# Performance work log

Measured on AMD Instinct MI355X. Metric: run time of the kernel, lower is better.

The kernel has to match this reference:

```python
import jax, jax.numpy as jnp
import numpy as np


def setup_inputs() -> dict:
    key = jax.random.key(0)
    k1, k2 = jax.random.split(key)
    B, S, D = 32, 1024, 384
    MAX_MEL_LEN = 8192  # >= max possible sum of durations (7*1024)
    x = jax.random.normal(k1, (B, S, D), dtype=jnp.float32)
    duration = jax.random.randint(k2, (B, S), 0, 8, dtype=jnp.int32)
    return {"x": x, "duration": duration, "max_mel_len": MAX_MEL_LEN}


def reference(x, duration, max_mel_len):
    # x: (B, S, D) float, duration: (B, S) int, max_mel_len: python int
    B, S, D = x.shape
    csum = jnp.cumsum(duration, axis=1)          # (B, S) inclusive cumsum
    mel_len = csum[:, -1]                        # (B,) expanded length per sample
    t = jnp.arange(max_mel_len, dtype=csum.dtype)  # (T,) output frame indices
    # frame t maps to token i where csum[i-1] <= t < csum[i]; side='right'
    # correctly skips zero-duration tokens (repeated csum values)
    idx = jax.vmap(lambda c: jnp.searchsorted(c, t, side='right'))(csum)  # (B, T)
    idx = jnp.clip(idx, 0, S - 1)
    out = jnp.take_along_axis(x, idx[:, :, None], axis=1)  # (B, T, D) gather
    mask = t[None, :] < mel_len[:, None]                   # (B, T) pad mask
    out = out * mask[:, :, None].astype(x.dtype)
    return out, mel_len.astype(jnp.int64)
```

## Files before the change

### kernel.cpp

```cpp
#include <hip/hip_runtime.h>


#define BATCH 32
#define SRC_S 1024
#define DIM   384
#define ROWS  32
#define C4    (DIM / 4)
#define NXCD  8

typedef float f32x4 __attribute__((ext_vector_type(4)));
typedef int   i32x4 __attribute__((ext_vector_type(4)));

__global__ __launch_bounds__(256)
void lr_fused_kernel(const f32x4* __restrict__ x4,
                     const int* __restrict__ duration,
                     f32x4* __restrict__ out4,
                     float* __restrict__ mel_out, int T) {
    __shared__ int wsum[4];
    __shared__ int src[ROWS];

    const int l = blockIdx.x;
    const int xcd = l & (NXCD - 1);
    const int j = l >> 3;
    const int b = xcd + NXCD * (j >> 8);
    const int t0 = (j & 255) * ROWS;
    const int tid = threadIdx.x;
    const int lane = tid & 63;
    const int wid = tid >> 6;

    if (tid < ROWS) src[tid] = -1;

    const i32x4 d = ((const i32x4*)(duration + b * SRC_S))[tid];
    const int s0 = d.x;
    const int s1 = s0 + d.y;
    const int s2 = s1 + d.z;
    const int s3 = s2 + d.w;
    int tot = s3;
    #pragma unroll
    for (int off = 1; off < 64; off <<= 1) {
        const int n = __shfl_up(tot, off, 64);
        if (lane >= off) tot += n;
    }
    if (lane == 63) wsum[wid] = tot;
    __syncthreads();
    int base = 0;
    #pragma unroll
    for (int w = 0; w < 3; ++w) base += (w < wid) ? wsum[w] : 0;
    const int mel_len = wsum[0] + wsum[1] + wsum[2] + wsum[3];
    const int pre = base + tot - s3;

    const int cs[4] = {pre + s0, pre + s1, pre + s2, pre + s3};
    const int st[4] = {pre, pre + s0, pre + s1, pre + s2};
    #pragma unroll
    for (int e = 0; e < 4; ++e) {
        const int lo = (st[e] > t0) ? st[e] : t0;
        const int hi = (cs[e] < t0 + ROWS) ? cs[e] : (t0 + ROWS);
        for (int t = lo; t < hi; ++t) src[t - t0] = tid * 4 + e;
    }
    __syncthreads();

    if (t0 == 0 && tid == 0) mel_out[b] = (float)mel_len;

    const f32x4* __restrict__ xb = x4 + (size_t)b * SRC_S * C4;
    f32x4* __restrict__ ob = out4 + ((size_t)b * T + t0) * C4;

    #pragma unroll
    for (int k = 0; k < (ROWS * C4) / 256; ++k) {
        const int i = tid + k * 256;
        const int row = i / C4;
        const int col = i - row * C4;
        const int sidx = src[row];
        f32x4 v = (f32x4)(0.f);
        if (sidx >= 0) v = xb[(size_t)sidx * C4 + col];
        __builtin_nontemporal_store(v, &ob[i]);
    }
}

extern "C" void kernel_launch(void* const* d_in, const int* in_sizes, int n_in,
                              void* d_out, int out_size, void* d_ws, size_t ws_size,
                              hipStream_t stream) {
    const float* x = (const float*)d_in[0];
    const int* duration = (const int*)d_in[1];
    const int T = (out_size - BATCH) / (BATCH * DIM);

    float* out = (float*)d_out;
    float* mel_out = out + (size_t)BATCH * T * DIM;

    const int nblocks = BATCH * (T / ROWS);
    lr_fused_kernel<<<nblocks, 256, 0, stream>>>((const f32x4*)x, duration,
                                                 (f32x4*)out, mel_out, T);
}
```

Measured before the change: 438.0 us.

## Split cumsum into separate kernel and skip padded tiles in gather

A small pre-kernel now computes the per-batch cumulative durations and mel lengths once, storing them in device globals. Previously every output tile redid the full 1024-element scan. The gather kernel reads the precomputed csum, writes zeros for tiles entirely past mel_len without any scan or sync, and stores precomputed row offsets in shared memory. Rows per block double to 64. The cost is an extra kernel launch and a global-memory round trip for csum. The block-to-batch mapping also hardcodes T=8192.

```diff
diff --git a/kernel.cpp b/kernel.cpp
--- a/kernel.cpp
+++ b/kernel.cpp
@@ -4,31 +4,23 @@
 #define BATCH 32
 #define SRC_S 1024
 #define DIM   384
-#define ROWS  32
+#define ROWS  64
 #define C4    (DIM / 4)
 #define NXCD  8
 
 typedef float f32x4 __attribute__((ext_vector_type(4)));
 typedef int   i32x4 __attribute__((ext_vector_type(4)));
 
+__device__ int g_csum[BATCH * SRC_S];
+__device__ int g_mel[BATCH];
+
 __global__ __launch_bounds__(256)
-void lr_fused_kernel(const f32x4* __restrict__ x4,
-                     const int* __restrict__ duration,
-                     f32x4* __restrict__ out4,
-                     float* __restrict__ mel_out, int T) {
+void lr_csum_kernel(const int* __restrict__ duration, float* __restrict__ mel_out) {
     __shared__ int wsum[4];
-    __shared__ int src[ROWS];
-
-    const int l = blockIdx.x;
-    const int xcd = l & (NXCD - 1);
-    const int j = l >> 3;
-    const int b = xcd + NXCD * (j >> 8);
-    const int t0 = (j & 255) * ROWS;
+    const int b = blockIdx.x;
     const int tid = threadIdx.x;
     const int lane = tid & 63;
     const int wid = tid >> 6;
-
-    if (tid < ROWS) src[tid] = -1;
 
     const i32x4 d = ((const i32x4*)(duration + b * SRC_S))[tid];
     const int s0 = d.x;
@@ -46,32 +38,68 @@
     int base = 0;
     #pragma unroll
     for (int w = 0; w < 3; ++w) base += (w < wid) ? wsum[w] : 0;
-    const int mel_len = wsum[0] + wsum[1] + wsum[2] + wsum[3];
     const int pre = base + tot - s3;
 
-    const int cs[4] = {pre + s0, pre + s1, pre + s2, pre + s3};
-    const int st[4] = {pre, pre + s0, pre + s1, pre + s2};
+    i32x4 c;
+    c.x = pre + s0; c.y = pre + s1; c.z = pre + s2; c.w = pre + s3;
+    ((i32x4*)(g_csum + b * SRC_S))[tid] = c;
+
+    if (tid == 255) {
+        const int mel = pre + s3;
+        g_mel[b] = mel;
+        mel_out[b] = (float)mel;
+    }
+}
+
+__global__ __launch_bounds__(256)
+void lr_gather_kernel(const f32x4* __restrict__ x4, f32x4* __restrict__ out4, int T) {
+    const int l = blockIdx.x;
+    const int xcd = l & (NXCD - 1);
+    const int j = l >> 3;
+    const int wpb = 8192 / ROWS;
+    const int b = xcd + NXCD * (j >> 7);
+    const int t0 = (j & (wpb - 1)) * ROWS;
+    const int tid = threadIdx.x;
+
+    f32x4* __restrict__ ob = out4 + ((size_t)b * T + t0) * C4;
+    const int mel = g_mel[b];
+
+    if (t0 >= mel) {
+        const f32x4 z = (f32x4)(0.f);
+        #pragma unroll
+        for (int k = 0; k < (ROWS * C4) / 256; ++k)
+            __builtin_nontemporal_store(z, &ob[tid + k * 256]);
+        return;
+    }
+
+    __shared__ int src[ROWS];
+    const int* __restrict__ cb = g_csum + b * SRC_S;
+    const i32x4 c = ((const i32x4*)cb)[tid];
+    const int prev = (tid == 0) ? 0 : cb[4 * tid - 1];
+
+    if (tid < ROWS) src[tid] = -1;
+    __syncthreads();
+
+    const int st[4] = {prev, c.x, c.y, c.z};
+    const int en[4] = {c.x, c.y, c.z, c.w};
     #pragma unroll
     for (int e = 0; e < 4; ++e) {
         const int lo = (st[e] > t0) ? st[e] : t0;
-        const int hi = (cs[e] < t0 + ROWS) ? cs[e] : (t0 + ROWS);
-        for (int t = lo; t < hi; ++t) src[t - t0] = tid * 4 + e;
+        const int hi = (en[e] < t0 + ROWS) ? en[e] : (t0 + ROWS);
+        const int off = (tid * 4 + e) * C4;
+        for (int t = lo; t < hi; ++t) src[t - t0] = off;
     }
     __syncthreads();
 
-    if (t0 == 0 && tid == 0) mel_out[b] = (float)mel_len;
-
     const f32x4* __restrict__ xb = x4 + (size_t)b * SRC_S * C4;
-    f32x4* __restrict__ ob = out4 + ((size_t)b * T + t0) * C4;
-
     #pragma unroll
     for (int k = 0; k < (ROWS * C4) / 256; ++k) {
         const int i = tid + k * 256;
         const int row = i / C4;
         const int col = i - row * C4;
-        const int sidx = src[row];
+        const int o = src[row];
         f32x4 v = (f32x4)(0.f);
-        if (sidx >= 0) v = xb[(size_t)sidx * C4 + col];
+        if (o >= 0) v = xb[o + col];
         __builtin_nontemporal_store(v, &ob[i]);
     }
 }
@@ -86,7 +114,9 @@
     float* out = (float*)d_out;
     float* mel_out = out + (size_t)BATCH * T * DIM;
 
+    lr_csum_kernel<<<BATCH, 256, 0, stream>>>(duration, mel_out);
+
     const int nblocks = BATCH * (T / ROWS);
-    lr_fused_kernel<<<nblocks, 256, 0, stream>>>((const f32x4*)x, duration,
-                                                 (f32x4*)out, mel_out, T);
+    lr_gather_kernel<<<nblocks, 256, 0, stream>>>((const f32x4*)x,
+                                                  (f32x4*)out, T);
 }
```

New measurement: 442.7 us. Within noise of the previous version (+1.1%).

## Split into index-table kernel plus flat gather sweep kernel

Applied to the files above, without the earlier changes.

Replaces the fused kernel, in which every block redoes the full per-batch prefix sum, with two kernels. The first computes the duration cumsum once per batch and writes a global source-offset table. The second does a flat, grid-strided gather sweep with 24 iterations per thread and plain stores instead of nontemporal ones. This removes the redundant per-block scans, at the cost of an extra launch, a global table round-trip, a serial per-thread table fill in only 32 blocks, and the loss of the XCD-aware block mapping.

```diff
diff --git a/kernel.cpp b/kernel.cpp
--- a/kernel.cpp
+++ b/kernel.cpp
@@ -4,31 +4,23 @@
 #define BATCH 32
 #define SRC_S 1024
 #define DIM   384
-#define ROWS  32
 #define C4    (DIM / 4)
-#define NXCD  8
+#define TMAX  8192
+#define NROW  (BATCH * TMAX)
 
 typedef float f32x4 __attribute__((ext_vector_type(4)));
 typedef int   i32x4 __attribute__((ext_vector_type(4)));
 
+__device__ int g_srcoff[NROW];
+
 __global__ __launch_bounds__(256)
-void lr_fused_kernel(const f32x4* __restrict__ x4,
-                     const int* __restrict__ duration,
-                     f32x4* __restrict__ out4,
-                     float* __restrict__ mel_out, int T) {
+void lr_table_kernel(const int* __restrict__ duration, float* __restrict__ mel_out,
+                     int T) {
     __shared__ int wsum[4];
-    __shared__ int src[ROWS];
-
-    const int l = blockIdx.x;
-    const int xcd = l & (NXCD - 1);
-    const int j = l >> 3;
-    const int b = xcd + NXCD * (j >> 8);
-    const int t0 = (j & 255) * ROWS;
+    const int b = blockIdx.x;
     const int tid = threadIdx.x;
     const int lane = tid & 63;
     const int wid = tid >> 6;
-
-    if (tid < ROWS) src[tid] = -1;
 
     const i32x4 d = ((const i32x4*)(duration + b * SRC_S))[tid];
     const int s0 = d.x;
@@ -46,33 +38,38 @@
     int base = 0;
     #pragma unroll
     for (int w = 0; w < 3; ++w) base += (w < wid) ? wsum[w] : 0;
-    const int mel_len = wsum[0] + wsum[1] + wsum[2] + wsum[3];
+    const int mel = wsum[0] + wsum[1] + wsum[2] + wsum[3];
     const int pre = base + tot - s3;
 
-    const int cs[4] = {pre + s0, pre + s1, pre + s2, pre + s3};
+    int* __restrict__ tb = g_srcoff + b * T;
+    const int xbase = b * SRC_S * C4;
     const int st[4] = {pre, pre + s0, pre + s1, pre + s2};
+    const int en[4] = {pre + s0, pre + s1, pre + s2, pre + s3};
     #pragma unroll
     for (int e = 0; e < 4; ++e) {
-        const int lo = (st[e] > t0) ? st[e] : t0;
-        const int hi = (cs[e] < t0 + ROWS) ? cs[e] : (t0 + ROWS);
-        for (int t = lo; t < hi; ++t) src[t - t0] = tid * 4 + e;
+        const int off = xbase + (tid * 4 + e) * C4;
+        for (int t = st[e]; t < en[e]; ++t) tb[t] = off;
     }
-    __syncthreads();
+    for (int t = mel + tid; t < T; t += 256) tb[t] = -1;
 
-    if (t0 == 0 && tid == 0) mel_out[b] = (float)mel_len;
+    if (tid == 0) mel_out[b] = (float)mel;
+}
 
-    const f32x4* __restrict__ xb = x4 + (size_t)b * SRC_S * C4;
-    f32x4* __restrict__ ob = out4 + ((size_t)b * T + t0) * C4;
+__global__ __launch_bounds__(256)
+void lr_sweep_kernel(const f32x4* __restrict__ x4, f32x4* __restrict__ out4,
+                     int iters) {
+    const int tid = threadIdx.x;
+    const int base = blockIdx.x * (iters * 256) + tid;
 
-    #pragma unroll
-    for (int k = 0; k < (ROWS * C4) / 256; ++k) {
-        const int i = tid + k * 256;
+    #pragma unroll 4
+    for (int k = 0; k < iters; ++k) {
+        const int i = base + k * 256;
         const int row = i / C4;
         const int col = i - row * C4;
-        const int sidx = src[row];
+        const int o = g_srcoff[row];
         f32x4 v = (f32x4)(0.f);
-        if (sidx >= 0) v = xb[(size_t)sidx * C4 + col];
-        __builtin_nontemporal_store(v, &ob[i]);
+        if (o >= 0) v = x4[o + col];
+        out4[i] = v;
     }
 }
 
@@ -86,7 +83,11 @@
     float* out = (float*)d_out;
     float* mel_out = out + (size_t)BATCH * T * DIM;
 
-    const int nblocks = BATCH * (T / ROWS);
-    lr_fused_kernel<<<nblocks, 256, 0, stream>>>((const f32x4*)x, duration,
-                                                 (f32x4*)out, mel_out, T);
+    lr_table_kernel<<<BATCH, 256, 0, stream>>>(duration, mel_out, T);
+
+    const int total = BATCH * T * C4;
+    const int iters = 24;
+    const int nblocks = total / (iters * 256);
+    lr_sweep_kernel<<<nblocks, 256, 0, stream>>>((const f32x4*)x,
+                                                 (f32x4*)out, iters);
 }
```

After: 460.5 us. 5.1% more time.
